# Performance work log

Measured on AMD Instinct MI355X. Metric: run time of the kernel, lower is better.

Reference implementation:

```python
import jax, jax.numpy as jnp
import numpy as np

DIM = 1024
HEADS = 16
HEAD_DIM = DIM // HEADS
SCALE = float(HEAD_DIM ** (-0.25))
ROPE_BASE = 10000.0


def apply_rope(x):
    # x: [B, N, H, D], rotate-half RoPE over last dim
    B, N, H, D = x.shape
    half = D // 2
    inv_freq = 1.0 / (ROPE_BASE ** (jnp.arange(half, dtype=jnp.float32) / half))
    freqs = jnp.arange(N, dtype=jnp.float32)[:, None] * inv_freq[None, :]  # [N, half]
    cos = jnp.cos(freqs)[None, :, None, :].astype(x.dtype)  # [1,N,1,half]
    sin = jnp.sin(freqs)[None, :, None, :].astype(x.dtype)
    x1, x2 = x[..., :half], x[..., half:]
    return jnp.concatenate([x1 * cos - x2 * sin, x1 * sin + x2 * cos], axis=-1)


def setup_inputs() -> dict:
    key = jax.random.key(0)
    k1, k2, k3 = jax.random.split(key, 3)
    x = jax.random.normal(k1, (4, 4096, DIM), dtype=jnp.float32)
    w_qkv = jax.random.normal(k2, (DIM, 3 * DIM), dtype=jnp.float32) * 0.02
    w_out = jax.random.normal(k3, (DIM, DIM), dtype=jnp.float32) * 0.02
    return {"x": x, "w_qkv": w_qkv, "w_out": w_out}


def reference(x, w_qkv, w_out):
    B, N, D = x.shape
    qkv = x @ w_qkv  # [B, N, 3*D]
    q, k, v = jnp.split(qkv, 3, axis=-1)
    q = q.reshape(B, N, HEADS, HEAD_DIM)
    k = k.reshape(B, N, HEADS, HEAD_DIM)
    v = v.reshape(B, N, HEADS, HEAD_DIM)
    q = apply_rope(q)
    k = apply_rope(k)
    # ELU(x*scale) + 1 feature map (positive)
    q = jax.nn.elu(q * SCALE) + 1.0
    k = jax.nn.elu(k * SCALE) + 1.0

    # sequential linear-attention recurrence over tokens (lax.scan)
    qT = jnp.moveaxis(q, 1, 0)  # [N, B, H, D]
    kT = jnp.moveaxis(k, 1, 0)
    vT = jnp.moveaxis(v, 1, 0)

    kv0 = jnp.zeros((B, HEADS, HEAD_DIM, HEAD_DIM), dtype=q.dtype)
    ks0 = jnp.zeros((B, HEADS, HEAD_DIM), dtype=q.dtype)

    def step(carry, qkv_t):
        kv, ks = carry
        qt, kt, vt = qkv_t
        kv = kv + jnp.einsum('bhd,bhm->bhdm', kt, vt)
        ks = ks + kt
        denom = jnp.maximum(jnp.einsum('bhd,bhd->bh', qt, ks), 1e-6)
        out_t = jnp.einsum('bhd,bhdm->bhm', qt, kv) / denom[..., None]
        return (kv, ks), out_t

    _, outT = jax.lax.scan(step, (kv0, ks0), (qT, kT, vT))  # outT: [N, B, H, D]
    out = jnp.moveaxis(outT, 0, 1).reshape(B, N, D)
    return out @ w_out
```

## Files before the change

kernel.cpp:

```cpp
#include <hip/hip_runtime.h>
#include <math.h>

#define BATCH 4
#define SEQ   4096
#define DMODEL 1024
#define HEADS 16
#define HDIM  64
#define CHUNK 64
#define NCHUNK 64
#define NTOK  16384
#define QKVC  3072
#define SCALE_F 0.35355339059327373f
#define ROPE_K 0.4152410118609203f

typedef unsigned short u16;
typedef _Float16 f16;
typedef __attribute__((ext_vector_type(8))) f16 f16x8;
typedef __attribute__((ext_vector_type(4))) float f32x4;

__device__ __forceinline__ u16 f2h(float f) { f16 h = (f16)f; return *(u16*)&h; }
__device__ __forceinline__ float h2f(u16 u) { f16 h = *(f16*)&u; return (float)h; }
__device__ __forceinline__ void storeC(u16* p, float v) { *p = f2h(v); }
__device__ __forceinline__ void storeC(float* p, float v) { *p = v; }

__device__ __forceinline__ void gload_lds16(const u16* g, u16* l)
{
    __builtin_amdgcn_global_load_lds(
        (const __attribute__((address_space(1))) void*)g,
        (__attribute__((address_space(3))) void*)l, 16, 0, 0);
}

#define BAR_STAGE(N) \
    asm volatile("s_waitcnt vmcnt(" #N ")" ::: "memory"); \
    __builtin_amdgcn_s_barrier(); \
    __builtin_amdgcn_sched_barrier(0);

#define BAR_END() \
    asm volatile("s_waitcnt lgkmcnt(0)" ::: "memory"); \
    __builtin_amdgcn_s_barrier(); \
    __builtin_amdgcn_sched_barrier(0);

__global__ __launch_bounds__(256)
void convert_f32_f16(const float* __restrict__ src, u16* __restrict__ dst)
{
    long i = ((long)blockIdx.x * 256 + threadIdx.x) * 4;
    float4 v = *(const float4*)(src + i);
    ushort4 o; o.x = f2h(v.x); o.y = f2h(v.y); o.z = f2h(v.z); o.w = f2h(v.w);
    *(ushort4*)(dst + i) = o;
}

__global__ __launch_bounds__(256)
void transpose_convert(const float* __restrict__ src, int C,
                       u16* __restrict__ dst, int dld)
{
    __shared__ u16 tile[64][72];
    const int r0 = blockIdx.y * 64, c0 = blockIdx.x * 64;
    const int t = threadIdx.x;
    const int rr = t >> 4, cc4 = (t & 15) * 4;
#pragma unroll
    for (int j = 0; j < 4; ++j) {
        int r = rr + j * 16;
        float4 v = *(const float4*)(src + (long)(r0 + r) * C + c0 + cc4);
        tile[cc4 + 0][r] = f2h(v.x);
        tile[cc4 + 1][r] = f2h(v.y);
        tile[cc4 + 2][r] = f2h(v.z);
        tile[cc4 + 3][r] = f2h(v.w);
    }
    __syncthreads();
#pragma unroll
    for (int j = 0; j < 4; ++j) {
        int c = rr + j * 16;
        ushort4 o = *(ushort4*)&tile[c][cc4];
        *(ushort4*)(dst + (long)(c0 + c) * dld + r0 + cc4) = o;
    }
}

template <typename CT, bool ROPE>
__global__ __launch_bounds__(512, 2)
void gemm_mfma(const u16* __restrict__ A, int lda,
               const u16* __restrict__ BT, int ldbt,
               CT* __restrict__ C, int ldc, int K)
{
    __shared__ u16 ringA[4][256 * 32];
    __shared__ u16 ringB[4][256 * 32];

    const int tid = threadIdx.x;
    const long m0 = (long)blockIdx.y * 256, n0 = (long)blockIdx.x * 256;
    const int w = tid >> 6, lane = tid & 63;
    const int wm = w >> 2, wn = w & 3;
    const int fr = lane & 15, quad = lane >> 4;
    const int sw = (quad ^ ((fr >> 1) & 3)) * 8;

    const int srow = tid >> 2;
    const int scol = ((tid & 3) ^ ((tid >> 3) & 3)) * 8;
    const u16* ga = A  + (m0 + srow) * (long)lda  + scol;
    const u16* gb = BT + (n0 + srow) * (long)ldbt + scol;
    const long a128 = 128 * (long)lda, b128 = 128 * (long)ldbt;

    f32x4 acc[8][4];
#pragma unroll
    for (int i = 0; i < 8; ++i)
#pragma unroll
        for (int j = 0; j < 4; ++j)
#pragma unroll
            for (int r = 0; r < 4; ++r) acc[i][j][r] = 0.0f;

    auto STAGE = [&](int h) {
        const int s = h & 3;
        u16* la = &ringA[s][w * 512];
        u16* lb = &ringB[s][w * 512];
        const long ko = (long)h << 5;
        gload_lds16(ga + ko,        la);
        gload_lds16(ga + ko + a128, la + 4096);
        gload_lds16(gb + ko,        lb);
        gload_lds16(gb + ko + b128, lb + 4096);
    };

    auto COMPUTE = [&](int h) {
        const u16* As_ = ringA[h & 3];
        const u16* Bs_ = ringB[h & 3];
        f16x8 af[8], bf[4];
#pragma unroll
        for (int mi = 0; mi < 8; ++mi)
            af[mi] = *(const f16x8*)&As_[(wm * 128 + mi * 16 + fr) * 32 + sw];
#pragma unroll
        for (int nj = 0; nj < 4; ++nj)
            bf[nj] = *(const f16x8*)&Bs_[(wn * 64 + nj * 16 + fr) * 32 + sw];
        __builtin_amdgcn_s_setprio(1);
#pragma unroll
        for (int mi = 0; mi < 8; ++mi)
#pragma unroll
            for (int nj = 0; nj < 4; ++nj)
                acc[mi][nj] = __builtin_amdgcn_mfma_f32_16x16x32_f16(
                    af[mi], bf[nj], acc[mi][nj], 0, 0, 0);
        __builtin_amdgcn_s_setprio(0);
    };

    const int NH = K >> 5;
    STAGE(0); STAGE(1); STAGE(2);
    for (int h = 0; h < NH - 3; ++h) {
        STAGE(h + 3);
        BAR_STAGE(12);
        COMPUTE(h);
        BAR_END();
    }
    BAR_STAGE(8);  COMPUTE(NH - 3);
    BAR_STAGE(4);  COMPUTE(NH - 2);
    BAR_STAGE(0);  COMPUTE(NH - 1);

    const long cm = m0 + wm * 128 + quad * 4;
    const long cn = n0 + wn * 64 + fr;

    if (ROPE && cn < 2048) {
        const float invf0 = exp2f(-(float)fr * ROPE_K);
        const float invf1 = exp2f(-(float)(fr + 16) * ROPE_K);
#pragma unroll
        for (int mi = 0; mi < 8; ++mi)
#pragma unroll
            for (int r = 0; r < 4; ++r) {
                long row = cm + mi * 16 + r;
                float n = (float)(int)(row & (SEQ - 1));
                float s0, c0, s1, c1;
                __sincosf(n * invf0, &s0, &c0);
                __sincosf(n * invf1, &s1, &c1);
                float x1 = acc[mi][0][r], x2 = acc[mi][2][r];
                float x3 = acc[mi][1][r], x4 = acc[mi][3][r];
                float u1 = (x1 * c0 - x2 * s0) * SCALE_F;
                float u2 = (x1 * s0 + x2 * c0) * SCALE_F;
                float u3 = (x3 * c1 - x4 * s1) * SCALE_F;
                float u4 = (x3 * s1 + x4 * c1) * SCALE_F;
                u1 = (u1 > 0.0f) ? (u1 + 1.0f) : __expf(u1);
                u2 = (u2 > 0.0f) ? (u2 + 1.0f) : __expf(u2);
                u3 = (u3 > 0.0f) ? (u3 + 1.0f) : __expf(u3);
                u4 = (u4 > 0.0f) ? (u4 + 1.0f) : __expf(u4);
                CT* pr = C + row * ldc + cn;
                storeC(pr, u1); storeC(pr + 16, u3);
                storeC(pr + 32, u2); storeC(pr + 48, u4);
            }
    } else {
#pragma unroll
        for (int mi = 0; mi < 8; ++mi)
#pragma unroll
            for (int nj = 0; nj < 4; ++nj)
#pragma unroll
                for (int r = 0; r < 4; ++r)
                    storeC(&C[(cm + mi * 16 + r) * ldc + cn + nj * 16], acc[mi][nj][r]);
    }
}

__global__ __launch_bounds__(256)
void chunk_sums_mfma(const u16* __restrict__ qkv,
                     u16* __restrict__ S, float* __restrict__ ksum)
{
    __shared__ u16 Kt[64][72];
    __shared__ u16 Vt[64][72];

    const int blk = blockIdx.x;
    const int c = blk & 63, bh = blk >> 6;
    const int b = bh >> 4, h = bh & 15;
    const int tid = threadIdx.x;
    const long base = (long)(b * SEQ + c * CHUNK) * QKVC + h * HDIM;

#pragma unroll
    for (int j = 0; j < 4; ++j) {
        int i4 = (j * 256 + tid) * 4;
        int t = i4 >> 6, d = i4 & 63;
        const u16* src = qkv + base + (long)t * QKVC + d;
        ushort4 kk = *(const ushort4*)(src + DMODEL);
        ushort4 vv = *(const ushort4*)(src + 2 * DMODEL);
        Kt[d + 0][t] = kk.x; Kt[d + 1][t] = kk.y;
        Kt[d + 2][t] = kk.z; Kt[d + 3][t] = kk.w;
        Vt[d + 0][t] = vv.x; Vt[d + 1][t] = vv.y;
        Vt[d + 2][t] = vv.z; Vt[d + 3][t] = vv.w;
    }
    __syncthreads();

    const int w = tid >> 6, lane = tid & 63;
    const int fr = lane & 15, quad = lane >> 4;

    f16x8 af0 = *(const f16x8*)&Vt[w * 16 + fr][quad * 8];
    f16x8 af1 = *(const f16x8*)&Vt[w * 16 + fr][32 + quad * 8];
    f32x4 acc[4];
#pragma unroll
    for (int j = 0; j < 4; ++j)
#pragma unroll
        for (int r = 0; r < 4; ++r) acc[j][r] = 0.0f;
#pragma unroll
    for (int j = 0; j < 4; ++j) {
        f16x8 b0 = *(const f16x8*)&Kt[j * 16 + fr][quad * 8];
        f16x8 b1 = *(const f16x8*)&Kt[j * 16 + fr][32 + quad * 8];
        acc[j] = __builtin_amdgcn_mfma_f32_16x16x32_f16(af0, b0, acc[j], 0, 0, 0);
        acc[j] = __builtin_amdgcn_mfma_f32_16x16x32_f16(af1, b1, acc[j], 0, 0, 0);
    }
    const long sb = (long)blk * 4096;
    const int mrow = w * 16 + quad * 4;
#pragma unroll
    for (int j = 0; j < 4; ++j)
#pragma unroll
        for (int r = 0; r < 4; ++r)
            S[sb + (mrow + r) * 64 + j * 16 + fr] = f2h(acc[j][r]);

    if (tid < 64) {
        float s = 0.0f;
        for (int t = 0; t < 64; ++t) s += h2f(Kt[tid][t]);
        ksum[(long)blk * 64 + tid] = s;
    }
}

__global__ __launch_bounds__(256)
void scan_kernel(u16* __restrict__ S, float* __restrict__ ksum)
{
    const int blk = blockIdx.x;
    const int slice = blk & 15, bh = blk >> 4;
    const int p = slice * 256 + threadIdx.x;
    const long base = (long)bh * NCHUNK * 4096 + p;
    float acc = 0.0f;
    for (int c = 0; c < NCHUNK; ++c) {
        long idx = base + (long)c * 4096;
        float tmp = h2f(S[idx]);
        S[idx] = f2h(acc);
        acc += tmp;
    }
    if (slice == 0 && threadIdx.x < 64) {
        const long kb = (long)bh * NCHUNK * 64 + threadIdx.x;
        float ka = 0.0f;
        for (int c = 0; c < NCHUNK; ++c) {
            float t = ksum[kb + (long)c * 64];
            ksum[kb + (long)c * 64] = ka;
            ka += t;
        }
    }
}

__global__ __launch_bounds__(256)
void chunk_out_mfma(u16* __restrict__ qkv,
                    const u16* __restrict__ S, const float* __restrict__ ksum)
{
    __shared__ u16 Qs[64][72];
    __shared__ u16 Ks[64][72];
    __shared__ u16 Vt[64][72];
    __shared__ u16 KVt[64][72];
    __shared__ u16 Sch[64][72];
    __shared__ float kss[64];
    __shared__ float den[64];

    const int blk = blockIdx.x;
    const int c = blk & 63, bh = blk >> 6;
    const int b = bh >> 4, h = bh & 15;
    const int tid = threadIdx.x;
    const long base = (long)(b * SEQ + c * CHUNK) * QKVC + h * HDIM;

#pragma unroll
    for (int j = 0; j < 4; ++j) {
        int i4 = (j * 256 + tid) * 4;
        int t = i4 >> 6, d = i4 & 63;
        const u16* src = qkv + base + (long)t * QKVC + d;
        *(ushort4*)&Qs[t][d] = *(const ushort4*)(src);
        *(ushort4*)&Ks[t][d] = *(const ushort4*)(src + DMODEL);
        ushort4 vv = *(const ushort4*)(src + 2 * DMODEL);
        Vt[d + 0][t] = vv.x; Vt[d + 1][t] = vv.y;
        Vt[d + 2][t] = vv.z; Vt[d + 3][t] = vv.w;
        *(ushort4*)&KVt[t][d] = *(const ushort4*)(S + (long)blk * 4096 + i4);
    }
    if (tid < 64) kss[tid] = ksum[(long)blk * 64 + tid];
    __syncthreads();

    const int w = tid >> 6, lane = tid & 63;
    const int fr = lane & 15, quad = lane >> 4;
    const int trow = w * 16 + quad * 4;

    f16x8 aq0 = *(const f16x8*)&Qs[w * 16 + fr][quad * 8];
    f16x8 aq1 = *(const f16x8*)&Qs[w * 16 + fr][32 + quad * 8];
    f32x4 sc[4];
#pragma unroll
    for (int j = 0; j < 4; ++j)
#pragma unroll
        for (int r = 0; r < 4; ++r) sc[j][r] = 0.0f;
#pragma unroll
    for (int j = 0; j < 4; ++j) {
        f16x8 b0 = *(const f16x8*)&Ks[j * 16 + fr][quad * 8];
        f16x8 b1 = *(const f16x8*)&Ks[j * 16 + fr][32 + quad * 8];
        sc[j] = __builtin_amdgcn_mfma_f32_16x16x32_f16(aq0, b0, sc[j], 0, 0, 0);
        sc[j] = __builtin_amdgcn_mfma_f32_16x16x32_f16(aq1, b1, sc[j], 0, 0, 0);
    }
#pragma unroll
    for (int j = 0; j < 4; ++j)
#pragma unroll
        for (int r = 0; r < 4; ++r) {
            int t = trow + r, s = j * 16 + fr;
            Sch[t][s] = f2h(s <= t ? sc[j][r] : 0.0f);
        }
    __syncthreads();

    if (tid < 64) {
        float dn = 0.0f;
        for (int d = 0; d < 64; ++d) dn += h2f(Qs[tid][d]) * kss[d];
        for (int s = 0; s <= tid; ++s) dn += h2f(Sch[tid][s]);
        den[tid] = 1.0f / fmaxf(dn, 1e-6f);
    }
    __syncthreads();

    f16x8 as0 = *(const f16x8*)&Sch[w * 16 + fr][quad * 8];
    f16x8 as1 = *(const f16x8*)&Sch[w * 16 + fr][32 + quad * 8];
    f32x4 oc[4];
#pragma unroll
    for (int j = 0; j < 4; ++j)
#pragma unroll
        for (int r = 0; r < 4; ++r) oc[j][r] = 0.0f;
#pragma unroll
    for (int j = 0; j < 4; ++j) {
        f16x8 b0 = *(const f16x8*)&Vt[j * 16 + fr][quad * 8];
        f16x8 b1 = *(const f16x8*)&Vt[j * 16 + fr][32 + quad * 8];
        oc[j] = __builtin_amdgcn_mfma_f32_16x16x32_f16(as0, b0, oc[j], 0, 0, 0);
        oc[j] = __builtin_amdgcn_mfma_f32_16x16x32_f16(as1, b1, oc[j], 0, 0, 0);
        f16x8 k0 = *(const f16x8*)&KVt[j * 16 + fr][quad * 8];
        f16x8 k1 = *(const f16x8*)&KVt[j * 16 + fr][32 + quad * 8];
        oc[j] = __builtin_amdgcn_mfma_f32_16x16x32_f16(aq0, k0, oc[j], 0, 0, 0);
        oc[j] = __builtin_amdgcn_mfma_f32_16x16x32_f16(aq1, k1, oc[j], 0, 0, 0);
    }
#pragma unroll
    for (int j = 0; j < 4; ++j)
#pragma unroll
        for (int r = 0; r < 4; ++r) {
            int t = trow + r;
            qkv[base + (long)t * QKVC + j * 16 + fr] = f2h(oc[j][r] * den[t]);
        }
}

extern "C" void kernel_launch(void* const* d_in, const int* in_sizes, int n_in,
                              void* d_out, int out_size, void* d_ws, size_t ws_size,
                              hipStream_t stream)
{
    const float* x     = (const float*)d_in[0];
    const float* w_qkv = (const float*)d_in[1];
    const float* w_out = (const float*)d_in[2];
    float* out = (float*)d_out;

    u16* qkv = (u16*)d_ws;
    u16* xf16  = (u16*)d_out;
    u16* wqkvT = xf16 + (size_t)NTOK * DMODEL;
    u16* S     = (u16*)d_out;
    float* ksum = (float*)((char*)d_out + 33554432);
    u16* woutT = qkv + 1024;

    dim3 blk(256);
    dim3 gblk(512);

    convert_f32_f16<<<NTOK * DMODEL / 1024, blk, 0, stream>>>(x, xf16);
    transpose_convert<<<dim3(QKVC / 64, DMODEL / 64), blk, 0, stream>>>(
        w_qkv, QKVC, wqkvT, DMODEL);

    gemm_mfma<u16, true><<<dim3(QKVC / 256, NTOK / 256), gblk, 0, stream>>>(
        xf16, DMODEL, wqkvT, DMODEL, qkv, QKVC, DMODEL);

    chunk_sums_mfma<<<64 * NCHUNK, blk, 0, stream>>>(qkv, S, ksum);
    scan_kernel<<<64 * 16, blk, 0, stream>>>(S, ksum);
    chunk_out_mfma<<<64 * NCHUNK, blk, 0, stream>>>(qkv, S, ksum);

    transpose_convert<<<dim3(DMODEL / 64, DMODEL / 64), blk, 0, stream>>>(
        w_out, DMODEL, woutT, QKVC);
    gemm_mfma<float, false><<<dim3(DMODEL / 256, NTOK / 256), gblk, 0, stream>>>(
        qkv, QKVC, woutT, QKVC, out, DMODEL, DMODEL);
}
```

Baseline: 380.7 us.

## Restructure GEMM main loop to one barrier per k-step with split MFMA halves

Rewrites the fp16 MFMA GEMM main loop so each k-step splits the A-fragment work into two halves. The next stage's A and B global-to-LDS loads are issued between the halves, and the wait plus barrier sit in the middle of the step. This replaces the previous two barriers per iteration (before and after compute) with a single barrier, aiming to overlap LDS reads, global loads and MFMAs better and cut synchronisation stalls. The tail vmcnt counts are handled explicitly per iteration, which adds branches and makes the ordering easy to get wrong.

New measurement: 356.6 us. 6.3% less time.

```diff
diff --git a/kernel.cpp b/kernel.cpp
--- a/kernel.cpp
+++ b/kernel.cpp
@@ -30,16 +30,6 @@
         (__attribute__((address_space(3))) void*)l, 16, 0, 0);
 }
 
-#define BAR_STAGE(N) \
-    asm volatile("s_waitcnt vmcnt(" #N ")" ::: "memory"); \
-    __builtin_amdgcn_s_barrier(); \
-    __builtin_amdgcn_sched_barrier(0);
-
-#define BAR_END() \
-    asm volatile("s_waitcnt lgkmcnt(0)" ::: "memory"); \
-    __builtin_amdgcn_s_barrier(); \
-    __builtin_amdgcn_sched_barrier(0);
-
 __global__ __launch_bounds__(256)
 void convert_f32_f16(const float* __restrict__ src, u16* __restrict__ dst)
 {
@@ -105,48 +95,74 @@
 #pragma unroll
             for (int r = 0; r < 4; ++r) acc[i][j][r] = 0.0f;
 
-    auto STAGE = [&](int h) {
-        const int s = h & 3;
-        u16* la = &ringA[s][w * 512];
-        u16* lb = &ringB[s][w * 512];
+    auto STAGE_A = [&](int h) {
+        u16* la = &ringA[h & 3][w * 512];
         const long ko = (long)h << 5;
         gload_lds16(ga + ko,        la);
         gload_lds16(ga + ko + a128, la + 4096);
+    };
+    auto STAGE_B = [&](int h) {
+        u16* lb = &ringB[h & 3][w * 512];
+        const long ko = (long)h << 5;
         gload_lds16(gb + ko,        lb);
         gload_lds16(gb + ko + b128, lb + 4096);
     };
 
-    auto COMPUTE = [&](int h) {
+    STAGE_A(0); STAGE_B(0);
+    STAGE_A(1); STAGE_B(1);
+    STAGE_A(2); STAGE_B(2);
+    asm volatile("s_waitcnt vmcnt(8)" ::: "memory");
+    __builtin_amdgcn_s_barrier();
+
+    const int NH = K >> 5;
+    for (int h = 0; h < NH; ++h) {
         const u16* As_ = ringA[h & 3];
         const u16* Bs_ = ringB[h & 3];
-        f16x8 af[8], bf[4];
-#pragma unroll
-        for (int mi = 0; mi < 8; ++mi)
-            af[mi] = *(const f16x8*)&As_[(wm * 128 + mi * 16 + fr) * 32 + sw];
+        f16x8 af0[4], af1[4], bf[4];
+
+#pragma unroll
+        for (int mi = 0; mi < 4; ++mi)
+            af0[mi] = *(const f16x8*)&As_[(wm * 128 + mi * 16 + fr) * 32 + sw];
 #pragma unroll
         for (int nj = 0; nj < 4; ++nj)
             bf[nj] = *(const f16x8*)&Bs_[(wn * 64 + nj * 16 + fr) * 32 + sw];
+        if (h < NH - 3) STAGE_A(h + 3);
+
         __builtin_amdgcn_s_setprio(1);
 #pragma unroll
-        for (int mi = 0; mi < 8; ++mi)
+        for (int mi = 0; mi < 4; ++mi)
 #pragma unroll
             for (int nj = 0; nj < 4; ++nj)
                 acc[mi][nj] = __builtin_amdgcn_mfma_f32_16x16x32_f16(
-                    af[mi], bf[nj], acc[mi][nj], 0, 0, 0);
+                    af0[mi], bf[nj], acc[mi][nj], 0, 0, 0);
         __builtin_amdgcn_s_setprio(0);
-    };
-
-    const int NH = K >> 5;
-    STAGE(0); STAGE(1); STAGE(2);
-    for (int h = 0; h < NH - 3; ++h) {
-        STAGE(h + 3);
-        BAR_STAGE(12);
-        COMPUTE(h);
-        BAR_END();
-    }
-    BAR_STAGE(8);  COMPUTE(NH - 3);
-    BAR_STAGE(4);  COMPUTE(NH - 2);
-    BAR_STAGE(0);  COMPUTE(NH - 1);
+
+#pragma unroll
+        for (int mi = 0; mi < 4; ++mi)
+            af1[mi] = *(const f16x8*)&As_[(wm * 128 + (mi + 4) * 16 + fr) * 32 + sw];
+        if (h < NH - 3) STAGE_B(h + 3);
+
+        if (h <= NH - 4) {
+            asm volatile("s_waitcnt vmcnt(8)" ::: "memory");
+        } else if (h == NH - 3) {
+            asm volatile("s_waitcnt vmcnt(4)" ::: "memory");
+        } else if (h == NH - 2) {
+            asm volatile("s_waitcnt vmcnt(0)" ::: "memory");
+        }
+        if (h < NH - 1) {
+            asm volatile("s_waitcnt lgkmcnt(0)" ::: "memory");
+            __builtin_amdgcn_s_barrier();
+        }
+
+        __builtin_amdgcn_s_setprio(1);
+#pragma unroll
+        for (int mi = 0; mi < 4; ++mi)
+#pragma unroll
+            for (int nj = 0; nj < 4; ++nj)
+                acc[mi + 4][nj] = __builtin_amdgcn_mfma_f32_16x16x32_f16(
+                    af1[mi], bf[nj], acc[mi + 4][nj], 0, 0, 0);
+        __builtin_amdgcn_s_setprio(0);
+    }
 
     const long cm = m0 + wm * 128 + quad * 4;
     const long cn = n0 + wn * 64 + fr;
```
